# Performance work log

Hardware: AMD Instinct MI355X
Metric: run time of the kernel (lower is better)

## Reference

```python
import jax, jax.numpy as jnp
import numpy as np

EMBED_DIM = 1024
VALUE_DIM = 2048
NUM_HEADS = 8
KEY_DIM = EMBED_DIM // NUM_HEADS      # 128
HEAD_DIM = VALUE_DIM // NUM_HEADS     # 256
B, T = 2, 2048
EPS = 1e-6


def _rotate_every_two(x):
    # x: [..., d] with d even; pairs (x0,x1)->(-x1,x0)
    x1 = x[..., ::2]
    x2 = x[..., 1::2]
    return jnp.stack((-x2, x1), axis=-1).reshape(x.shape)


def _theta_shift(x, sin, cos):
    # sin/cos: [T, key_dim] broadcast over [B, H, T, key_dim]
    return x * cos + _rotate_every_two(x) * sin


def setup_inputs() -> dict:
    key = jax.random.key(0)
    ks = jax.random.split(key, 6)
    x = jax.random.normal(ks[0], (B, T, EMBED_DIM), dtype=jnp.float32)

    # rotary angles as in torchscale RetNetRelPos
    angle = 1.0 / (10000.0 ** jnp.linspace(0.0, 1.0, KEY_DIM // 2))
    angle = jnp.repeat(angle, 2)                       # [key_dim], interleaved pairs
    idx = jnp.arange(T, dtype=jnp.float32)
    sin = jnp.sin(idx[:, None] * angle[None, :])       # [T, key_dim]
    cos = jnp.cos(idx[:, None] * angle[None, :])

    # per-head decay mask, normalized by sqrt(row-sum) as in RetNet
    decay = jnp.log(1.0 - 2.0 ** (-5.0 - jnp.arange(NUM_HEADS, dtype=jnp.float32)))
    diff = idx[:, None] - idx[None, :]                 # [T, T]
    exponent = jnp.where(diff >= 0, decay[:, None, None] * diff[None], -jnp.inf)
    mask = jnp.exp(exponent)                           # [H, T, T], lower-triangular decay
    mask = mask / jnp.sqrt(mask.sum(-1, keepdims=True))

    s = 0.02
    Wq = s * jax.random.normal(ks[1], (EMBED_DIM, EMBED_DIM), dtype=jnp.float32)
    Wk = s * jax.random.normal(ks[2], (EMBED_DIM, EMBED_DIM), dtype=jnp.float32)
    Wv = s * jax.random.normal(ks[3], (EMBED_DIM, VALUE_DIM), dtype=jnp.float32)
    Wg = s * jax.random.normal(ks[4], (EMBED_DIM, VALUE_DIM), dtype=jnp.float32)
    Wo = s * jax.random.normal(ks[5], (VALUE_DIM, EMBED_DIM), dtype=jnp.float32)
    return {"x": x, "sin": sin, "cos": cos, "mask": mask,
            "Wq": Wq, "Wk": Wk, "Wv": Wv, "Wg": Wg, "Wo": Wo}


def reference(x, sin, cos, mask, Wq, Wk, Wv, Wg, Wo):
    bsz, tgt_len, _ = x.shape
    scaling = KEY_DIM ** (-0.5)

    q = x @ Wq
    k = (x @ Wk) * scaling
    v = x @ Wv
    g = x @ Wg

    q = q.reshape(bsz, tgt_len, NUM_HEADS, KEY_DIM).transpose(0, 2, 1, 3)  # [B,H,T,kd]
    k = k.reshape(bsz, tgt_len, NUM_HEADS, KEY_DIM).transpose(0, 2, 1, 3)
    qr = _theta_shift(q, sin, cos)
    kr = _theta_shift(k, sin, cos)

    vr = v.reshape(bsz, tgt_len, NUM_HEADS, HEAD_DIM).transpose(0, 2, 1, 3)  # [B,H,T,hd]

    # parallel retention: decay-masked QK^T with abs-sum normalization (detached)
    qk = jnp.einsum('bhtd,bhsd->bhts', qr, kr) * mask[None]
    denom = jnp.clip(jnp.sum(jnp.abs(jax.lax.stop_gradient(qk)), axis=-1, keepdims=True),
                     1.0, 50000.0)
    qk = qk / denom
    out = jnp.einsum('bhts,bhsd->bhtd', qk, vr)          # [B,H,T,hd]
    out = out.transpose(0, 2, 1, 3)                      # [B,T,H,hd]

    # per-head RMSNorm (no affine)
    out = out * jax.lax.rsqrt(jnp.mean(out * out, axis=-1, keepdims=True) + EPS)
    out = out.reshape(bsz, tgt_len, VALUE_DIM)

    out = jax.nn.silu(g) * out
    return out @ Wo
```

## Files before the change

### kernel.cpp

```cpp
#include <hip/hip_runtime.h>
#include <hip/hip_bf16.h>
#include <math.h>

constexpr int T_SEQ = 2048;
constexpr int BB    = 2;
constexpr int EMBED = 1024;
constexpr int VDIM  = 2048;
constexpr int NHEADS = 8;
constexpr int KDIM  = 128;
constexpr int HDIM  = 256;
constexpr int ROWS  = BB * T_SEQ;
constexpr float EPS = 1e-6f;

typedef float  f32x4  __attribute__((ext_vector_type(4)));
typedef __bf16 bf16x8 __attribute__((ext_vector_type(8)));
typedef __bf16 bf16x4 __attribute__((ext_vector_type(4)));

__device__ __forceinline__ void gload16(const void* g, void* l) {
    __builtin_amdgcn_global_load_lds(
        (__attribute__((address_space(1))) void*)g,
        (__attribute__((address_space(3))) void*)l, 16, 0, 0);
}

#define WAITV(n) asm volatile("s_waitcnt vmcnt(" #n ")" ::: "memory")
#define BARRIER() __builtin_amdgcn_s_barrier()

__global__ __launch_bounds__(256)
void prep_all(const float* __restrict__ x, const float* __restrict__ Wq,
              const float* __restrict__ Wk, const float* __restrict__ Wv,
              const float* __restrict__ Wg, const float* __restrict__ Wo,
              __bf16* __restrict__ xb,
              __bf16* __restrict__ WqT, __bf16* __restrict__ WkT,
              __bf16* __restrict__ WvT, __bf16* __restrict__ WgT,
              __bf16* __restrict__ WoT) {
    const int bid = blockIdx.x;
    const int x_ = threadIdx.x, y_ = threadIdx.y;
    if (bid >= 8192) {
        const int i = (bid - 8192) * 256 + y_ * 32 + x_;
        float4 v = reinterpret_cast<const float4*>(x)[i];
        bf16x4 o = { (__bf16)v.x, (__bf16)v.y, (__bf16)v.z, (__bf16)v.w };
        reinterpret_cast<bf16x4*>(xb)[i] = o;
        return;
    }
    const float* W; __bf16* WT; int K, N, cx, cy;
    if (bid < 1024)      { W = Wq; WT = WqT; K = 1024; N = 1024; int rm = bid;        cx = rm & 31; cy = rm >> 5; }
    else if (bid < 2048) { W = Wk; WT = WkT; K = 1024; N = 1024; int rm = bid - 1024; cx = rm & 31; cy = rm >> 5; }
    else if (bid < 4096) { W = Wv; WT = WvT; K = 1024; N = 2048; int rm = bid - 2048; cx = rm & 63; cy = rm >> 6; }
    else if (bid < 6144) { W = Wg; WT = WgT; K = 1024; N = 2048; int rm = bid - 4096; cx = rm & 63; cy = rm >> 6; }
    else                 { W = Wo; WT = WoT; K = 2048; N = 1024; int rm = bid - 6144; cx = rm & 31; cy = rm >> 5; }

    __shared__ float tile[32][33];
    const int c0 = cx * 32, k0 = cy * 32;
    #pragma unroll
    for (int p = 0; p < 4; ++p)
        tile[y_ + p * 8][x_] = W[(size_t)(k0 + y_ + p * 8) * N + c0 + x_];
    __syncthreads();
    #pragma unroll
    for (int p = 0; p < 4; ++p)
        WT[(size_t)(c0 + y_ + p * 8) * K + k0 + x_] = (__bf16)tile[x_][y_ + p * 8];
}

__global__ __launch_bounds__(256)
void gemm_qk(const __bf16* __restrict__ A, const __bf16* __restrict__ BT,
             __bf16* __restrict__ Qb, __bf16* __restrict__ Kb,
             const float* __restrict__ sinT, const float* __restrict__ cosT) {
    constexpr int K = EMBED;
    __shared__ __align__(16) char smem[32768];
    __bf16* As = (__bf16*)smem;
    __bf16* Bs = (__bf16*)(smem + 16384);

    const int bid = blockIdx.x;
    const int rr = bid >> 3;
    const int bx = (bid & 7) * 2 + (rr & 1);
    const int by = rr >> 1;
    const int rowBase = by * 128;
    const int colBase = bx * 128;

    const int tid = threadIdx.x;
    const int w = tid >> 6, lane = tid & 63;
    const int g = lane >> 4, r = lane & 15;
    const int wm = w >> 1, wn = w & 1;

    const int vr  = lane >> 3;
    const int swz = ((lane & 7) ^ vr) * 8;
    const __bf16* aSb = A  + (size_t)(rowBase + 32 * w + vr) * K + swz;
    const __bf16* bSb = BT + (size_t)(colBase + 32 * w + vr) * K + swz;

    f32x4 acc[4][4];
    #pragma unroll
    for (int i = 0; i < 4; ++i)
        #pragma unroll
        for (int j = 0; j < 4; ++j)
            acc[i][j] = (f32x4){0.f, 0.f, 0.f, 0.f};

    for (int k0 = 0; k0 < K; k0 += 64) {
        __syncthreads();
        #pragma unroll
        for (int p = 0; p < 4; ++p) {
            const int cc = 4 * w + p;
            gload16(aSb + (size_t)(8 * p) * K + k0, smem         + cc * 1024);
            gload16(bSb + (size_t)(8 * p) * K + k0, smem + 16384 + cc * 1024);
        }
        __syncthreads();

        #pragma unroll
        for (int kk = 0; kk < 2; ++kk) {
            bf16x8 bfrag[4];
            #pragma unroll
            for (int nf = 0; nf < 4; ++nf) {
                const int row = wn * 64 + nf * 16 + r;
                bfrag[nf] = *reinterpret_cast<const bf16x8*>(
                    &Bs[row * 64 + (((kk << 2) + g) ^ (r & 7)) * 8]);
            }
            #pragma unroll
            for (int mf = 0; mf < 4; ++mf) {
                const int row = wm * 64 + mf * 16 + r;
                bf16x8 a = *reinterpret_cast<const bf16x8*>(
                    &As[row * 64 + (((kk << 2) + g) ^ (r & 7)) * 8]);
                #pragma unroll
                for (int nf = 0; nf < 4; ++nf)
                    acc[mf][nf] = __builtin_amdgcn_mfma_f32_16x16x32_bf16(a, bfrag[nf], acc[mf][nf], 0, 0, 0);
            }
        }
    }

    constexpr float kscale = 0.08838834764831845f;
    __bf16* dst; int cofs; float alphaSeg;
    if (colBase < 1024) { dst = Qb; cofs = colBase;        alphaSeg = 1.0f;   }
    else                { dst = Kb; cofs = colBase - 1024; alphaSeg = kscale; }

    #pragma unroll
    for (int mf = 0; mf < 4; ++mf)
        #pragma unroll
        for (int nf = 0; nf < 4; ++nf)
            #pragma unroll
            for (int j = 0; j < 4; ++j) {
                const int row  = rowBase + wm * 64 + mf * 16 + g * 4 + j;
                const int colL = cofs + wn * 64 + nf * 16 + r;
                float v = acc[mf][nf][j] * alphaSeg;
                const float p = __shfl_xor(v, 1);
                const int t  = row & (T_SEQ - 1);
                const int dh = colL & (KDIM - 1);
                const float c = cosT[t * KDIM + dh];
                const float s = sinT[t * KDIM + dh];
                v = (r & 1) ? (v * c + p * s) : (v * c - p * s);
                dst[(size_t)row * 1024 + colL] = (__bf16)v;
            }
}

#define STAGEH(ISB, TAU, HF) do { \
    const __bf16* s_ = ((ISB) ? BT : A) + \
        (size_t)((((ISB) ? colBase : rowBase)) + (HF) * 128 + w * 8 + srow) * 1024 + \
        (TAU) * 64 + swz; \
    char* d_ = smem + ((ISB) ? 65536 : 0) + (((TAU) & 1) * 2 + (HF)) * 16384 + w * 1024; \
    gload16(s_, d_); \
    gload16(s_ + (size_t)64 * 1024, d_ + 8192); \
} while (0)

#define QPHASE(TAU, Q, STGSTMT) do { \
    const int p_ = (TAU) & 1; \
    const __bf16* Ab_ = (const __bf16*)(smem + (p_ * 2 + wm) * 16384); \
    const __bf16* Bb_ = (const __bf16*)(smem + 65536 + (p_ * 2 + bh) * 16384); \
    if ((Q) == 0) { \
        _Pragma("unroll") for (int nf = 0; nf < 4; ++nf) \
        _Pragma("unroll") for (int kk = 0; kk < 2; ++kk) \
            bq[nf][kk] = *(const bf16x8*)(Bb_ + (bro + nf * 16) * 64 + ((kk * 4 + g) ^ rx) * 8); \
    } \
    bf16x8 aq_[2][2]; \
    _Pragma("unroll") for (int i = 0; i < 2; ++i) \
    _Pragma("unroll") for (int kk = 0; kk < 2; ++kk) \
        aq_[i][kk] = *(const bf16x8*)(Ab_ + (((Q) * 2 + i) * 16 + r) * 64 + ((kk * 4 + g) ^ rx) * 8); \
    STGSTMT; \
    BARRIER(); \
    __builtin_amdgcn_s_setprio(1); \
    _Pragma("unroll") for (int i = 0; i < 2; ++i) \
    _Pragma("unroll") for (int nf = 0; nf < 4; ++nf) \
    _Pragma("unroll") for (int kk = 0; kk < 2; ++kk) \
        acc[(Q) * 2 + i][nf] = __builtin_amdgcn_mfma_f32_16x16x32_bf16( \
            aq_[i][kk], bq[nf][kk], acc[(Q) * 2 + i][nf], 0, 0, 0); \
    __builtin_amdgcn_s_setprio(0); \
} while (0)

__global__ __launch_bounds__(512, 2)
void gemm_vg(const __bf16* __restrict__ A, const __bf16* __restrict__ BT,
             __bf16* __restrict__ Vt, __bf16* __restrict__ Gb) {
    __shared__ __align__(16) char smem[131072];

    const int bid = blockIdx.x;
    const int j2 = bid >> 3;
    const int bxA = (bid & 7) * 2 + (j2 & 1);
    const int by  = j2 >> 1;
    const int rowBase = by * 256;
    const int colBase = 2048 + bxA * 256;

    const int tid = threadIdx.x;
    const int w = tid >> 6, lane = tid & 63;
    const int g = lane >> 4, r = lane & 15;
    const int wm = w >> 2, wn = w & 3;
    const int rx = r & 7;
    const int bh = wn >> 1;
    const int bro = (wn & 1) * 64 + r;

    const int srow = lane >> 3;
    const int swz  = ((lane & 7) ^ srow) * 8;

    f32x4 acc[8][4];
    #pragma unroll
    for (int i = 0; i < 8; ++i)
        #pragma unroll
        for (int j = 0; j < 4; ++j)
            acc[i][j] = (f32x4){0.f, 0.f, 0.f, 0.f};
    bf16x8 bq[4][2];

    STAGEH(1, 0, 0); STAGEH(1, 0, 1);
    STAGEH(0, 0, 0); STAGEH(0, 0, 1);
    STAGEH(1, 1, 0); STAGEH(1, 1, 1);
    WAITV(4);
    BARRIER();

    for (int it = 0; it < 8; ++it) {
        const int e = 2 * it, o = e + 1;
        const bool more = (it < 7);
        QPHASE(e, 0, STAGEH(0, o, 0));                        BARRIER();
        QPHASE(e, 1, STAGEH(0, o, 1));                        BARRIER();
        QPHASE(e, 2, if (more) STAGEH(1, e + 2, 0));          BARRIER();
        QPHASE(e, 3, if (more) STAGEH(1, e + 2, 1));
        if (more) { WAITV(4); } else { WAITV(0); }            BARRIER();
        QPHASE(o, 0, if (more) STAGEH(0, e + 2, 0));          BARRIER();
        QPHASE(o, 1, if (more) STAGEH(0, e + 2, 1));          BARRIER();
        QPHASE(o, 2, if (more) STAGEH(1, o + 2, 0));          BARRIER();
        QPHASE(o, 3, if (more) STAGEH(1, o + 2, 1));
        if (more) { WAITV(4); } else { WAITV(0); }            BARRIER();
    }

    if (bxA < 8) {
        __bf16* Es = (__bf16*)smem + w * 4608;
        const int colV0 = (colBase - 2048) + wn * 64;
        const int h = colV0 >> 8, dd0 = colV0 & 255;
        const int li = lane & 7, rgrp = lane >> 3;
        #pragma unroll
        for (int h2 = 0; h2 < 2; ++h2) {
            #pragma unroll
            for (int mf = 0; mf < 4; ++mf)
                #pragma unroll
                for (int nf = 0; nf < 4; ++nf) {
                    f32x4 a = acc[h2 * 4 + mf][nf];
                    bf16x4 v = { (__bf16)a[0], (__bf16)a[1], (__bf16)a[2], (__bf16)a[3] };
                    *reinterpret_cast<bf16x4*>(&Es[(nf * 16 + r) * 72 + mf * 16 + g * 4]) = v;
                }
            __syncthreads();
            const int t0g = rowBase + wm * 128 + h2 * 64;
            const int bq_ = t0g >> 11, tl = t0g & 2047;
            __bf16* vtb = Vt + ((size_t)(bq_ * NHEADS + h) * HDIM + dd0) * T_SEQ + tl;
            #pragma unroll
            for (int c = 0; c < 8; ++c) {
                const int drow = 8 * c + rgrp;
                bf16x8 v = *reinterpret_cast<const bf16x8*>(&Es[drow * 72 + li * 8]);
                *reinterpret_cast<bf16x8*>(vtb + (size_t)drow * T_SEQ + li * 8) = v;
            }
            __syncthreads();
        }
        return;
    }

    const int cofs = colBase - 4096;
    #pragma unroll
    for (int mf = 0; mf < 8; ++mf)
        #pragma unroll
        for (int nf = 0; nf < 4; ++nf)
            #pragma unroll
            for (int j = 0; j < 4; ++j) {
                const int row  = rowBase + wm * 128 + mf * 16 + g * 4 + j;
                const int colL = cofs + wn * 64 + nf * 16 + r;
                Gb[(size_t)row * 2048 + colL] = (__bf16)acc[mf][nf][j];
            }
}

__global__ __launch_bounds__(256)
void gemm_wo(const __bf16* __restrict__ A, const __bf16* __restrict__ BT,
             float* __restrict__ C) {
    constexpr int N = EMBED, K = VDIM;
    __shared__ __align__(16) char smem[24576];
    __bf16* As = (__bf16*)smem;
    __bf16* Bs = (__bf16*)(smem + 8192);

    const int bid = blockIdx.x;
    const int swzb = (bid & 7) * 64 + (bid >> 3);
    const int rowBase = (swzb >> 3) * 64;
    const int colBase = (swzb & 7) * 128;

    const int tid = threadIdx.x;
    const int w = tid >> 6, lane = tid & 63;
    const int g = lane >> 4, r = lane & 15;
    const int wm = w >> 1, wn = w & 1;

    const int vr  = lane >> 3;
    const int swz = ((lane & 7) ^ vr) * 8;
    const __bf16* aSb = A  + (size_t)(rowBase + 16 * w + vr) * K + swz;
    const __bf16* bSb = BT + (size_t)(colBase + 32 * w + vr) * K + swz;

    f32x4 acc[2][4];
    #pragma unroll
    for (int i = 0; i < 2; ++i)
        #pragma unroll
        for (int j = 0; j < 4; ++j)
            acc[i][j] = (f32x4){0.f, 0.f, 0.f, 0.f};

    for (int k0 = 0; k0 < K; k0 += 64) {
        __syncthreads();
        #pragma unroll
        for (int p = 0; p < 2; ++p) {
            const int cc = 2 * w + p;
            gload16(aSb + (size_t)(8 * p) * K + k0, smem + cc * 1024);
        }
        #pragma unroll
        for (int p = 0; p < 4; ++p) {
            const int cc = 4 * w + p;
            gload16(bSb + (size_t)(8 * p) * K + k0, smem + 8192 + cc * 1024);
        }
        __syncthreads();

        #pragma unroll
        for (int kk = 0; kk < 2; ++kk) {
            bf16x8 bfrag[4];
            #pragma unroll
            for (int nf = 0; nf < 4; ++nf) {
                const int row = wn * 64 + nf * 16 + r;
                bfrag[nf] = *reinterpret_cast<const bf16x8*>(
                    &Bs[row * 64 + (((kk << 2) + g) ^ (r & 7)) * 8]);
            }
            #pragma unroll
            for (int mf = 0; mf < 2; ++mf) {
                const int row = wm * 32 + mf * 16 + r;
                bf16x8 a = *reinterpret_cast<const bf16x8*>(
                    &As[row * 64 + (((kk << 2) + g) ^ (r & 7)) * 8]);
                #pragma unroll
                for (int nf = 0; nf < 4; ++nf)
                    acc[mf][nf] = __builtin_amdgcn_mfma_f32_16x16x32_bf16(a, bfrag[nf], acc[mf][nf], 0, 0, 0);
            }
        }
    }

    #pragma unroll
    for (int mf = 0; mf < 2; ++mf)
        #pragma unroll
        for (int nf = 0; nf < 4; ++nf)
            #pragma unroll
            for (int j = 0; j < 4; ++j) {
                const int row = rowBase + wm * 32 + mf * 16 + g * 4 + j;
                const int col = colBase + wn * 64 + nf * 16 + r;
                C[(size_t)row * N + col] = acc[mf][nf][j];
            }
}

__global__ __launch_bounds__(256)
void retention_mfma(const __bf16* __restrict__ Qb, const __bf16* __restrict__ Kb,
                    const __bf16* __restrict__ Vt,
                    const __bf16* __restrict__ Gb, __bf16* __restrict__ Yb) {
    const int tid = threadIdx.x;
    const int w = tid >> 6, lane = tid & 63;
    const int g = lane >> 4, r = lane & 15;
    const int rx = r & 7;
    const int bid = blockIdx.x;
    const int h = bid & 7;
    const int slot = bid >> 3;
    const int b = slot & 1;
    const int x = slot >> 1;
    const int qt = (b == 0) ? (31 - x) : x;
    const int tt0 = qt * 64;
    const int trow0 = w * 16;

    __shared__ __align__(16) __bf16 Ks[2][64][128];
    __shared__ __align__(16) __bf16 Vs[256][64];
    __shared__ __align__(16) __bf16 Ps[4][16][72];

    const float rho   = 1.0f - exp2f(-(float)(5 + h));
    const float l2r   = log2f(rho);
    const float inv1m = exp2f((float)(5 + h));
    int   tj[4];
    float nrm[4];
    #pragma unroll
    for (int j = 0; j < 4; ++j) {
        tj[j] = tt0 + trow0 + g * 4 + j;
        nrm[j] = rsqrtf((1.0f - exp2f(l2r * (float)(tj[j] + 1))) * inv1m);
    }
    float pneg[4];
    #pragma unroll
    for (int ssub = 0; ssub < 4; ++ssub)
        pneg[ssub] = exp2f(-l2r * (float)(ssub * 16 + r));

    bf16x8 qf[4];
    {
        const __bf16* qrow = Qb + ((size_t)(b * T_SEQ + tt0 + trow0 + r)) * EMBED + h * KDIM;
        #pragma unroll
        for (int kb = 0; kb < 4; ++kb)
            qf[kb] = *reinterpret_cast<const bf16x8*>(qrow + kb * 32 + g * 8);
    }

    f32x4 acc[16];
    #pragma unroll
    for (int db = 0; db < 16; ++db) acc[db] = (f32x4){0.f, 0.f, 0.f, 0.f};
    float dsum[4] = {0.f, 0.f, 0.f, 0.f};

    const __bf16* vtbase = Vt + ((size_t)(b * NHEADS + h) * HDIM) * T_SEQ;
    const __bf16* kbase  = Kb + ((size_t)(b * T_SEQ)) * EMBED + h * KDIM;

    const int klr = lane >> 4;
    const int kc  = lane & 15;
    const int kswz_even = (kc ^ klr) * 8;
    const int kswz_odd  = (kc ^ (4 + klr)) * 8;
    const int vlr  = lane >> 3;
    const int vswz = ((lane & 7) ^ vlr) * 8;

    #pragma unroll
    for (int p = 0; p < 4; ++p) {
        const int cc = 4 * w + p;
        const int se = (p & 1) ? kswz_odd : kswz_even;
        gload16(kbase + (size_t)(4 * cc + klr) * EMBED + se,
                (char*)&Ks[0][0][0] + cc * 1024);
    }

    int cur = 0;
    const int nS = qt + 1;
    for (int st = 0; st < nS; ++st) {
        const int ss0 = st * 64;
        WAITV(0);
        BARRIER();

        #pragma unroll
        for (int p = 0; p < 8; ++p) {
            const int cc = 8 * w + p;
            gload16(vtbase + (size_t)(8 * cc + vlr) * T_SEQ + ss0 + vswz,
                    (char*)&Vs[0][0] + cc * 1024);
        }
        const bool more = (st + 1 < nS);
        if (more) {
            const int ssn = ss0 + 64;
            #pragma unroll
            for (int p = 0; p < 4; ++p) {
                const int cc = 4 * w + p;
                const int se = (p & 1) ? kswz_odd : kswz_even;
                gload16(kbase + (size_t)(ssn + 4 * cc + klr) * EMBED + se,
                        (char*)&Ks[cur ^ 1][0][0] + cc * 1024);
            }
        }

        float wj[4];
        #pragma unroll
        for (int j = 0; j < 4; ++j)
            wj[j] = exp2f(l2r * (float)(tj[j] - ss0)) * nrm[j];
        const bool diag = (st == qt);

        #pragma unroll
        for (int ssub = 0; ssub < 4; ++ssub) {
            f32x4 sacc = (f32x4){0.f, 0.f, 0.f, 0.f};
            #pragma unroll
            for (int kb = 0; kb < 4; ++kb) {
                bf16x8 kf = *reinterpret_cast<const bf16x8*>(
                    &Ks[cur][ssub * 16 + r][((kb * 4 + g) ^ rx) * 8]);
                sacc = __builtin_amdgcn_mfma_f32_16x16x32_bf16(qf[kb], kf, sacc, 0, 0, 0);
            }
            const int scol = ss0 + ssub * 16 + r;
            const float mfac = pneg[ssub];
            #pragma unroll
            for (int j = 0; j < 4; ++j) {
                float pv = sacc[j] * (wj[j] * mfac);
                if (diag && scol > tj[j]) pv = 0.f;
                dsum[j] += fabsf(pv);
                Ps[w][g * 4 + j][ssub * 16 + r] = (__bf16)pv;
            }
        }

        if (more) { WAITV(4); } else { WAITV(0); }
        BARRIER();

        #pragma unroll
        for (int sh = 0; sh < 2; ++sh) {
            bf16x8 pf = *reinterpret_cast<const bf16x8*>(&Ps[w][r][sh * 32 + g * 8]);
            #pragma unroll
            for (int db = 0; db < 16; ++db) {
                bf16x8 vf = *reinterpret_cast<const bf16x8*>(
                    &Vs[db * 16 + r][((sh * 4 + g) ^ rx) * 8]);
                acc[db] = __builtin_amdgcn_mfma_f32_16x16x32_bf16(pf, vf, acc[db], 0, 0, 0);
            }
        }
        cur ^= 1;
    }

    #pragma unroll
    for (int j = 0; j < 4; ++j) {
        float v = dsum[j];
        v += __shfl_xor(v, 1); v += __shfl_xor(v, 2);
        v += __shfl_xor(v, 4); v += __shfl_xor(v, 8);
        dsum[j] = fminf(fmaxf(v, 1.0f), 50000.0f);
    }
    float ss[4] = {0.f, 0.f, 0.f, 0.f};
    #pragma unroll
    for (int db = 0; db < 16; ++db)
        #pragma unroll
        for (int j = 0; j < 4; ++j) {
            const float v = acc[db][j] / dsum[j];
            acc[db][j] = v;
            ss[j] = fmaf(v, v, ss[j]);
        }
    #pragma unroll
    for (int j = 0; j < 4; ++j) {
        float v = ss[j];
        v += __shfl_xor(v, 1); v += __shfl_xor(v, 2);
        v += __shfl_xor(v, 4); v += __shfl_xor(v, 8);
        ss[j] = rsqrtf(v * (1.0f / 256.0f) + EPS);
    }
    #pragma unroll
    for (int j = 0; j < 4; ++j) {
        const size_t row = (size_t)(b * T_SEQ + tj[j]);
        const __bf16* grow = Gb + row * VDIM + h * HDIM;
        __bf16* yrow = Yb + row * VDIM + h * HDIM;
        #pragma unroll
        for (int db = 0; db < 16; ++db) {
            const int c = db * 16 + r;
            const float gv = (float)grow[c];
            const float sil = gv / (1.0f + expf(-gv));
            yrow[c] = (__bf16)(sil * acc[db][j] * ss[j]);
        }
    }
}

extern "C" void kernel_launch(void* const* d_in, const int* in_sizes, int n_in,
                              void* d_out, int out_size, void* d_ws, size_t ws_size,
                              hipStream_t stream) {
    (void)in_sizes; (void)n_in; (void)out_size; (void)ws_size;

    const float* x    = (const float*)d_in[0];
    const float* sinT = (const float*)d_in[1];
    const float* cosT = (const float*)d_in[2];
    const float* Wq   = (const float*)d_in[4];
    const float* Wk   = (const float*)d_in[5];
    const float* Wv   = (const float*)d_in[6];
    const float* Wg   = (const float*)d_in[7];
    const float* Wo   = (const float*)d_in[8];
    float* out = (float*)d_out;

    char* wsp = (char*)d_ws;
    __bf16* xb  = (__bf16*)(wsp);
    __bf16* WqT = (__bf16*)(wsp + (8u  << 20));
    __bf16* WkT = (__bf16*)(wsp + (10u << 20));
    __bf16* WvT = (__bf16*)(wsp + (12u << 20));
    __bf16* WgT = (__bf16*)(wsp + (16u << 20));
    __bf16* WoT = (__bf16*)(wsp + (20u << 20));
    __bf16* Qb  = (__bf16*)(wsp + (24u << 20));
    __bf16* Kb  = (__bf16*)(wsp + (32u << 20));
    __bf16* Yb  = (__bf16*)(wsp + (40u << 20));
    __bf16* Gb  = (__bf16*)(wsp + (56u << 20));
    __bf16* Vt  = (__bf16*)(wsp + (72u << 20));
    __bf16* WTall = WqT;

    const dim3 blk(256);
    const dim3 tblk(32, 8);

    prep_all<<<12288, tblk, 0, stream>>>(x, Wq, Wk, Wv, Wg, Wo,
                                         xb, WqT, WkT, WvT, WgT, WoT);

    gemm_qk<<<512, blk, 0, stream>>>(xb, WTall, Qb, Kb, sinT, cosT);

    gemm_vg<<<256, 512, 0, stream>>>(xb, WTall, Vt, Gb);

    retention_mfma<<<512, blk, 0, stream>>>(Qb, Kb, Vt, Gb, Yb);

    gemm_wo<<<512, blk, 0, stream>>>(Yb, WoT, out);
}
```

Baseline: 172.4 us.

## Split long causal query tiles across two blocks and merge with a combine kernel

Query tiles in the upper half of the sequence are now split along the key dimension into two blocks. Each writes its unnormalized partial output (bf16) and partial abs-sums to workspace, and a new combine kernel sums them, applies the clamp, RMSNorm and SiLU gating. This is meant to even out the triangular causal workload so no block has to walk all 32 key tiles. In exchange it adds an extra launch, a global write and read of the partials, and some rounding from storing partials in bf16. The partial buffers reuse workspace regions that held the bf16 weights, which are no longer needed at that point.

```diff
diff --git a/kernel.cpp b/kernel.cpp
--- a/kernel.cpp
+++ b/kernel.cpp
@@ -356,17 +356,26 @@
 __global__ __launch_bounds__(256)
 void retention_mfma(const __bf16* __restrict__ Qb, const __bf16* __restrict__ Kb,
                     const __bf16* __restrict__ Vt,
-                    const __bf16* __restrict__ Gb, __bf16* __restrict__ Yb) {
+                    const __bf16* __restrict__ Gb, __bf16* __restrict__ Yb,
+                    __bf16* __restrict__ PA, float* __restrict__ PD) {
     const int tid = threadIdx.x;
     const int w = tid >> 6, lane = tid & 63;
     const int g = lane >> 4, r = lane & 15;
     const int rx = r & 7;
     const int bid = blockIdx.x;
     const int h = bid & 7;
-    const int slot = bid >> 3;
-    const int b = slot & 1;
-    const int x = slot >> 1;
-    const int qt = (b == 0) ? (31 - x) : x;
+    const int u = bid >> 3;
+    int b, qt, sBeg, sEnd, pIdx;
+    if (u < 32) {
+        b = u & 1; qt = 15 - (u >> 1); sBeg = 0; sEnd = qt + 1; pIdx = -1;
+    } else {
+        const int v = u & 31;
+        b = v & 1; qt = 16 + (v >> 1);
+        const int nS = qt + 1, mid = (nS + 1) >> 1;
+        const int half = (u >= 64) ? 1 : 0;
+        sBeg = half ? mid : 0; sEnd = half ? nS : mid;
+        pIdx = (((b * 8 + h) * 16) + (qt - 16)) * 2 + half;
+    }
     const int tt0 = qt * 64;
     const int trow0 = w * 16;
 
@@ -416,13 +425,12 @@
     for (int p = 0; p < 4; ++p) {
         const int cc = 4 * w + p;
         const int se = (p & 1) ? kswz_odd : kswz_even;
-        gload16(kbase + (size_t)(4 * cc + klr) * EMBED + se,
+        gload16(kbase + (size_t)(sBeg * 64 + 4 * cc + klr) * EMBED + se,
                 (char*)&Ks[0][0][0] + cc * 1024);
     }
 
     int cur = 0;
-    const int nS = qt + 1;
-    for (int st = 0; st < nS; ++st) {
+    for (int st = sBeg; st < sEnd; ++st) {
         const int ss0 = st * 64;
         WAITV(0);
         BARRIER();
@@ -433,7 +441,7 @@
             gload16(vtbase + (size_t)(8 * cc + vlr) * T_SEQ + ss0 + vswz,
                     (char*)&Vs[0][0] + cc * 1024);
         }
-        const bool more = (st + 1 < nS);
+        const bool more = (st + 1 < sEnd);
         if (more) {
             const int ssn = ss0 + 64;
             #pragma unroll
@@ -492,8 +500,30 @@
         float v = dsum[j];
         v += __shfl_xor(v, 1); v += __shfl_xor(v, 2);
         v += __shfl_xor(v, 4); v += __shfl_xor(v, 8);
-        dsum[j] = fminf(fmaxf(v, 1.0f), 50000.0f);
-    }
+        dsum[j] = v;
+    }
+
+    if (pIdx >= 0) {
+        float* pd = PD + (size_t)pIdx * 64;
+        if (r == 0) {
+            #pragma unroll
+            for (int j = 0; j < 4; ++j)
+                pd[trow0 + g * 4 + j] = dsum[j];
+        }
+        __bf16* pa = PA + (size_t)pIdx * (64 * 256);
+        #pragma unroll
+        for (int j = 0; j < 4; ++j) {
+            __bf16* prow = pa + (trow0 + g * 4 + j) * 256;
+            #pragma unroll
+            for (int db = 0; db < 16; ++db)
+                prow[db * 16 + r] = (__bf16)acc[db][j];
+        }
+        return;
+    }
+
+    #pragma unroll
+    for (int j = 0; j < 4; ++j)
+        dsum[j] = fminf(fmaxf(dsum[j], 1.0f), 50000.0f);
     float ss[4] = {0.f, 0.f, 0.f, 0.f};
     #pragma unroll
     for (int db = 0; db < 16; ++db)
@@ -522,6 +552,56 @@
             const float sil = gv / (1.0f + expf(-gv));
             yrow[c] = (__bf16)(sil * acc[db][j] * ss[j]);
         }
+    }
+}
+
+__global__ __launch_bounds__(256)
+void retention_combine(const __bf16* __restrict__ PA, const float* __restrict__ PD,
+                       const __bf16* __restrict__ Gb, __bf16* __restrict__ Yb) {
+    const int cb = blockIdx.x;
+    const int qti = cb & 15, h = (cb >> 4) & 7, b = cb >> 7;
+    const int qt = 16 + qti;
+    const int tid = threadIdx.x;
+    const int lr = tid >> 2;
+    const int cq = tid & 3;
+
+    const __bf16* a0 = PA + (size_t)(cb * 2)     * 16384 + lr * 256 + cq * 64;
+    const __bf16* a1 = PA + (size_t)(cb * 2 + 1) * 16384 + lr * 256 + cq * 64;
+    float dt = PD[(cb * 2) * 64 + lr] + PD[(cb * 2 + 1) * 64 + lr];
+    dt = fminf(fmaxf(dt, 1.0f), 50000.0f);
+    const float inv = 1.0f / dt;
+
+    float v[64];
+    float ssp = 0.f;
+    #pragma unroll
+    for (int i = 0; i < 8; ++i) {
+        bf16x8 x0 = *reinterpret_cast<const bf16x8*>(a0 + i * 8);
+        bf16x8 x1 = *reinterpret_cast<const bf16x8*>(a1 + i * 8);
+        #pragma unroll
+        for (int e = 0; e < 8; ++e) {
+            const float s = ((float)x0[e] + (float)x1[e]) * inv;
+            v[i * 8 + e] = s;
+            ssp = fmaf(s, s, ssp);
+        }
+    }
+    ssp += __shfl_xor(ssp, 1);
+    ssp += __shfl_xor(ssp, 2);
+    const float rs = rsqrtf(ssp * (1.0f / 256.0f) + EPS);
+
+    const size_t row = (size_t)(b * T_SEQ + qt * 64 + lr);
+    const __bf16* grow = Gb + row * VDIM + h * HDIM + cq * 64;
+    __bf16* yrow = Yb + row * VDIM + h * HDIM + cq * 64;
+    #pragma unroll
+    for (int i = 0; i < 8; ++i) {
+        bf16x8 gv8 = *reinterpret_cast<const bf16x8*>(grow + i * 8);
+        bf16x8 o;
+        #pragma unroll
+        for (int e = 0; e < 8; ++e) {
+            const float gv = (float)gv8[e];
+            const float sil = gv / (1.0f + expf(-gv));
+            o[e] = (__bf16)(sil * v[i * 8 + e] * rs);
+        }
+        *reinterpret_cast<bf16x8*>(yrow + i * 8) = o;
     }
 }
 
@@ -553,6 +633,8 @@
     __bf16* Gb  = (__bf16*)(wsp + (56u << 20));
     __bf16* Vt  = (__bf16*)(wsp + (72u << 20));
     __bf16* WTall = WqT;
+    __bf16* PA  = (__bf16*)(wsp);
+    float*  PD  = (float*)(wsp + (16u << 20));
 
     const dim3 blk(256);
     const dim3 tblk(32, 8);
@@ -564,7 +646,9 @@
 
     gemm_vg<<<256, 512, 0, stream>>>(xb, WTall, Vt, Gb);
 
-    retention_mfma<<<512, blk, 0, stream>>>(Qb, Kb, Vt, Gb, Yb);
+    retention_mfma<<<768, blk, 0, stream>>>(Qb, Kb, Vt, Gb, Yb, PA, PD);
+
+    retention_combine<<<256, blk, 0, stream>>>(PA, PD, Gb, Yb);
 
     gemm_wo<<<512, blk, 0, stream>>>(Yb, WoT, out);
 }
```

New measurement: 178.1 us. 1.03x slower.

## Load K and V fragments directly from global memory instead of LDS

Applied to the files above, without the earlier changes.

Drops the shared-memory double-buffered staging of K and V tiles in the retention kernel and reads MFMA operand fragments directly from global memory, removing block-wide barriers and waitcnts. This is meant to cut LDS traffic and synchronisation overhead. In exchange, each wave independently re-fetches the same K/V data through the cache hierarchy. Load latency is no longer hidden by asynchronous prefetch.

```diff
diff --git a/kernel.cpp b/kernel.cpp
--- a/kernel.cpp
+++ b/kernel.cpp
@@ -360,7 +360,6 @@
     const int tid = threadIdx.x;
     const int w = tid >> 6, lane = tid & 63;
     const int g = lane >> 4, r = lane & 15;
-    const int rx = r & 7;
     const int bid = blockIdx.x;
     const int h = bid & 7;
     const int slot = bid >> 3;
@@ -370,8 +369,6 @@
     const int tt0 = qt * 64;
     const int trow0 = w * 16;
 
-    __shared__ __align__(16) __bf16 Ks[2][64][128];
-    __shared__ __align__(16) __bf16 Vs[256][64];
     __shared__ __align__(16) __bf16 Ps[4][16][72];
 
     const float rho   = 1.0f - exp2f(-(float)(5 + h));
@@ -402,48 +399,12 @@
     for (int db = 0; db < 16; ++db) acc[db] = (f32x4){0.f, 0.f, 0.f, 0.f};
     float dsum[4] = {0.f, 0.f, 0.f, 0.f};
 
-    const __bf16* vtbase = Vt + ((size_t)(b * NHEADS + h) * HDIM) * T_SEQ;
-    const __bf16* kbase  = Kb + ((size_t)(b * T_SEQ)) * EMBED + h * KDIM;
-
-    const int klr = lane >> 4;
-    const int kc  = lane & 15;
-    const int kswz_even = (kc ^ klr) * 8;
-    const int kswz_odd  = (kc ^ (4 + klr)) * 8;
-    const int vlr  = lane >> 3;
-    const int vswz = ((lane & 7) ^ vlr) * 8;
-
-    #pragma unroll
-    for (int p = 0; p < 4; ++p) {
-        const int cc = 4 * w + p;
-        const int se = (p & 1) ? kswz_odd : kswz_even;
-        gload16(kbase + (size_t)(4 * cc + klr) * EMBED + se,
-                (char*)&Ks[0][0][0] + cc * 1024);
-    }
-
-    int cur = 0;
+    const __bf16* kfb = Kb + ((size_t)(b * T_SEQ + r)) * EMBED + h * KDIM + g * 8;
+    const __bf16* vfb = Vt + ((size_t)((b * NHEADS + h) * HDIM) + r) * T_SEQ + g * 8;
+
     const int nS = qt + 1;
     for (int st = 0; st < nS; ++st) {
         const int ss0 = st * 64;
-        WAITV(0);
-        BARRIER();
-
-        #pragma unroll
-        for (int p = 0; p < 8; ++p) {
-            const int cc = 8 * w + p;
-            gload16(vtbase + (size_t)(8 * cc + vlr) * T_SEQ + ss0 + vswz,
-                    (char*)&Vs[0][0] + cc * 1024);
-        }
-        const bool more = (st + 1 < nS);
-        if (more) {
-            const int ssn = ss0 + 64;
-            #pragma unroll
-            for (int p = 0; p < 4; ++p) {
-                const int cc = 4 * w + p;
-                const int se = (p & 1) ? kswz_odd : kswz_even;
-                gload16(kbase + (size_t)(ssn + 4 * cc + klr) * EMBED + se,
-                        (char*)&Ks[cur ^ 1][0][0] + cc * 1024);
-            }
-        }
 
         float wj[4];
         #pragma unroll
@@ -457,7 +418,7 @@
             #pragma unroll
             for (int kb = 0; kb < 4; ++kb) {
                 bf16x8 kf = *reinterpret_cast<const bf16x8*>(
-                    &Ks[cur][ssub * 16 + r][((kb * 4 + g) ^ rx) * 8]);
+                    kfb + (size_t)(ss0 + ssub * 16) * EMBED + kb * 32);
                 sacc = __builtin_amdgcn_mfma_f32_16x16x32_bf16(qf[kb], kf, sacc, 0, 0, 0);
             }
             const int scol = ss0 + ssub * 16 + r;
@@ -471,20 +432,16 @@
             }
         }
 
-        if (more) { WAITV(4); } else { WAITV(0); }
-        BARRIER();
-
         #pragma unroll
         for (int sh = 0; sh < 2; ++sh) {
             bf16x8 pf = *reinterpret_cast<const bf16x8*>(&Ps[w][r][sh * 32 + g * 8]);
             #pragma unroll
             for (int db = 0; db < 16; ++db) {
                 bf16x8 vf = *reinterpret_cast<const bf16x8*>(
-                    &Vs[db * 16 + r][((sh * 4 + g) ^ rx) * 8]);
+                    vfb + (size_t)(db * 16) * T_SEQ + ss0 + sh * 32);
                 acc[db] = __builtin_amdgcn_mfma_f32_16x16x32_bf16(pf, vf, acc[db], 0, 0, 0);
             }
         }
-        cur ^= 1;
     }
 
     #pragma unroll
```

Result: slower. 370.5 us (+114.9%).
